# Performance work log

Hardware: AMD Instinct MI355X
Metric: run time of the kernel (lower is better)

The kernel has to match this reference:

```python
import jax, jax.numpy as jnp
import numpy as np
from jax import lax

B = 64
FEAT = 512
SEED_DIM = 128
NUM_PC = 256
NPART = 4096
NFPS = 512


def setup_inputs() -> dict:
    key = jax.random.key(0)
    ks = jax.random.split(key, 32)
    s = 0.02
    rn = lambda k, shape: jax.random.normal(k, shape, jnp.float32) * s
    inp = {}
    inp["feat"] = jax.random.normal(ks[0], (B, FEAT, 1), jnp.float32)
    inp["patch_xyz"] = jax.random.normal(ks[1], (B, 3, 128), jnp.float32)
    inp["patch_feat"] = jax.random.normal(ks[2], (B, FEAT, 128), jnp.float32)
    inp["partial"] = jax.random.normal(ks[3], (B, NPART, 3), jnp.float32)
    # ConvTranspose1d(512, 128, 256): weight [in, out, k]
    inp["ps_w"] = rn(ks[4], (FEAT, 128, NUM_PC))
    inp["ps_b"] = jnp.zeros((128,), jnp.float32)
    # MLP_Res(in, hidden, out): conv1 [hid,in], conv2 [out,hid], shortcut [out,in]
    def mlp_res_params(k, din, dhid, dout):
        k1, k2, k3 = jax.random.split(k, 3)
        return (rn(k1, (dhid, din)), jnp.zeros((dhid,), jnp.float32),
                rn(k2, (dout, dhid)), jnp.zeros((dout,), jnp.float32),
                rn(k3, (dout, din)), jnp.zeros((dout,), jnp.float32))
    (inp["m1_w1"], inp["m1_b1"], inp["m1_w2"], inp["m1_b2"], inp["m1_ws"], inp["m1_bs"]) = mlp_res_params(ks[5], FEAT + 128, 128, 128)
    (inp["m2_w1"], inp["m2_b1"], inp["m2_w2"], inp["m2_b2"], inp["m2_ws"], inp["m2_bs"]) = mlp_res_params(ks[6], 128, 64, 128)
    (inp["m3_w1"], inp["m3_b1"], inp["m3_w2"], inp["m3_b2"], inp["m3_ws"], inp["m3_bs"]) = mlp_res_params(ks[7], FEAT + 128, 128, SEED_DIM)
    inp["m4_w1"] = rn(ks[8], (64, SEED_DIM))
    inp["m4_b1"] = jnp.zeros((64,), jnp.float32)
    inp["m4_w2"] = rn(ks[9], (3, 64))
    inp["m4_b2"] = jnp.zeros((3,), jnp.float32)
    return inp


def _conv1(w, b, x):
    # 1x1 Conv1d: w [out,in], x [B,in,N] -> [B,out,N]
    return jnp.einsum('oi,bin->bon', w, x) + b[None, :, None]


def _mlp_res(x, w1, b1, w2, b2, ws, bs):
    h = jax.nn.relu(_conv1(w1, b1, x))
    return _conv1(w2, b2, h) + _conv1(ws, bs, x)


def _fps(xyz, npoint):
    # farthest point sampling (PointNet++ semantics, start at index 0)
    # xyz: [B, N, 3] -> [B, npoint, 3]
    Bb, N, _ = xyz.shape
    dist0 = jnp.full((Bb, N), 1e10, dtype=xyz.dtype)
    far0 = jnp.zeros((Bb,), jnp.int32)

    def step(carry, _):
        dist, far = carry
        centroid = jnp.take_along_axis(xyz, far[:, None, None], axis=1)  # [B,1,3]
        d = jnp.sum((xyz - centroid) ** 2, axis=-1)  # [B,N]
        dist = jnp.minimum(dist, d)
        new_far = jnp.argmax(dist, axis=-1).astype(jnp.int32)
        return (dist, new_far), far

    _, idxs = lax.scan(step, (dist0, far0), None, length=npoint)  # [npoint, B]
    idxs = idxs.T  # [B, npoint]
    return jnp.take_along_axis(xyz, idxs[..., None], axis=1)


def reference(feat, patch_xyz, patch_feat, partial,
              ps_w, ps_b,
              m1_w1, m1_b1, m1_w2, m1_b2, m1_ws, m1_bs,
              m2_w1, m2_b1, m2_w2, m2_b2, m2_ws, m2_bs,
              m3_w1, m3_b1, m3_w2, m3_b2, m3_ws, m3_bs,
              m4_w1, m4_b1, m4_w2, m4_b2):
    # ConvTranspose1d on length-1 input: [B,C,1] x [C,O,K] -> [B,O,K]
    x1 = jnp.einsum('bc,cok->bok', feat[:, :, 0], ps_w) + ps_b[None, :, None]
    feat_r = jnp.broadcast_to(feat, (feat.shape[0], feat.shape[1], NUM_PC))
    x1 = _mlp_res(jnp.concatenate([x1, feat_r], axis=1), m1_w1, m1_b1, m1_w2, m1_b2, m1_ws, m1_bs)
    x2 = _mlp_res(x1, m2_w1, m2_b1, m2_w2, m2_b2, m2_ws, m2_bs)
    x3 = _mlp_res(jnp.concatenate([x2, feat_r], axis=1), m3_w1, m3_b1, m3_w2, m3_b2, m3_ws, m3_bs)
    seed = _conv1(m4_w2, m4_b2, jax.nn.relu(_conv1(m4_w1, m4_b1, x3)))  # [B,3,256]
    all_pts = jnp.concatenate([seed.transpose(0, 2, 1), partial], axis=1)  # [B,256+N,3]
    x = _fps(all_pts, NFPS).transpose(0, 2, 1)  # [B,3,512]
    return (seed, x3, x)
```

## Files before the change

kernel.cpp:

```cpp
#include <hip/hip_runtime.h>
#include <stdint.h>

#define X3_OFF 49152
#define FPS_OFF 2146304


__global__ void k_prep(const float* __restrict__ feat, float* __restrict__ ws) {
    int g = blockIdx.x * 256 + threadIdx.x;
    int c = g >> 6, b = g & 63;
    ws[32768 + c * 64 + b] = feat[b * 512 + c];
}

__global__ void k_tterms(const float* __restrict__ w1, const float* __restrict__ ws1,
                         const float* __restrict__ w3, const float* __restrict__ ws3,
                         float* __restrict__ ws) {
    int g = blockIdx.x * 256 + threadIdx.x;
    int which = g >> 13;
    int o = (g >> 6) & 127;
    int b = g & 63;
    const float* W = (which == 0) ? w1 : (which == 1) ? ws1
                     : (which == 2) ? w3 : ws3;
    const float* ft = ws + 32768;
    float acc = 0.f;
#pragma unroll 4
    for (int c = 0; c < 512; ++c)
        acc = fmaf(W[o * 640 + 128 + c], ft[c * 64 + b], acc);
    ws[which * 8192 + o * 64 + b] = acc;
}

__global__ void k_deconv(const float* __restrict__ psw,
                         const float* __restrict__ psb,
                         const float* __restrict__ ws,
                         float* __restrict__ stage) {
    int n = blockIdx.x * 256 + threadIdx.x;
    int b0 = blockIdx.y * 16;
    const float* featT = ws + 32768;
    float acc[16];
    float bias = psb[n >> 8];
#pragma unroll
    for (int j = 0; j < 16; ++j) acc[j] = bias;
    for (int c = 0; c < 512; ++c) {
        float pw = psw[c * 32768 + n];
#pragma unroll
        for (int j = 0; j < 16; ++j)
            acc[j] = fmaf(pw, featT[c * 64 + b0 + j], acc[j]);
    }
#pragma unroll
    for (int j = 0; j < 16; ++j)
        stage[(b0 + j) * 32768 + n] = acc[j];
}

__device__ __forceinline__ void gemm8(const float* __restrict__ Wg, int ld, int o0,
                                      const float* S, int K, float acc[8], int lane) {
#pragma unroll 4
    for (int i = 0; i < K; ++i) {
        float x = S[i * 64 + lane];
#pragma unroll
        for (int r = 0; r < 8; ++r)
            acc[r] = fmaf(x, Wg[(o0 + r) * ld + i], acc[r]);
    }
}

struct FusedW {
    const float *m1_w1, *m1_b1, *m1_w2, *m1_b2, *m1_ws, *m1_bs;
    const float *m2_w1, *m2_b1, *m2_w2, *m2_b2, *m2_ws, *m2_bs;
    const float *m3_w1, *m3_b1, *m3_w2, *m3_b2, *m3_ws, *m3_bs;
    const float *m4_w1, *m4_b1, *m4_w2, *m4_b2;
};

__global__ void __launch_bounds__(512)
k_fused(FusedW P, const float* __restrict__ ws, float* __restrict__ fout) {
    int b  = blockIdx.x >> 2;
    int k0 = (blockIdx.x & 3) * 64;
    int lane = threadIdx.x & 63;
    int wave = __builtin_amdgcn_readfirstlane(threadIdx.x >> 6);

    const float* T1  = ws;
    const float* T1s = ws + 8192;
    const float* T3  = ws + 16384;
    const float* T3s = ws + 24576;
    float* stage = fout + X3_OFF + b * 32768;

    __shared__ float Xs[8192];
    __shared__ float Hs[8192];

#pragma unroll
    for (int s = 0; s < 16; ++s) {
        int e = threadIdx.x + s * 512;
        int o = e >> 6, kk = e & 63;
        Xs[e] = stage[o * 256 + k0 + kk];
    }
    __syncthreads();

    float yreg[2][8];

#pragma unroll
    for (int half = 0; half < 2; ++half) {
        int o0 = wave * 16 + half * 8;
        float acc[8];
#pragma unroll
        for (int r = 0; r < 8; ++r) acc[r] = T1[(o0 + r) * 64 + b] + P.m1_b1[o0 + r];
        gemm8(P.m1_w1, 640, o0, Xs, 128, acc, lane);
#pragma unroll
        for (int r = 0; r < 8; ++r) Hs[(o0 + r) * 64 + lane] = fmaxf(acc[r], 0.f);
    }
    __syncthreads();
#pragma unroll
    for (int half = 0; half < 2; ++half) {
        int o0 = wave * 16 + half * 8;
        float acc[8];
#pragma unroll
        for (int r = 0; r < 8; ++r)
            acc[r] = T1s[(o0 + r) * 64 + b] + P.m1_b2[o0 + r] + P.m1_bs[o0 + r];
        gemm8(P.m1_w2, 128, o0, Hs, 128, acc, lane);
        gemm8(P.m1_ws, 640, o0, Xs, 128, acc, lane);
#pragma unroll
        for (int r = 0; r < 8; ++r) yreg[half][r] = acc[r];
    }
    __syncthreads();
#pragma unroll
    for (int half = 0; half < 2; ++half) {
        int o0 = wave * 16 + half * 8;
#pragma unroll
        for (int r = 0; r < 8; ++r) Xs[(o0 + r) * 64 + lane] = yreg[half][r];
    }
    __syncthreads();

    {
        int o0 = wave * 8;
        float acc[8];
#pragma unroll
        for (int r = 0; r < 8; ++r) acc[r] = P.m2_b1[o0 + r];
        gemm8(P.m2_w1, 128, o0, Xs, 128, acc, lane);
#pragma unroll
        for (int r = 0; r < 8; ++r) Hs[(o0 + r) * 64 + lane] = fmaxf(acc[r], 0.f);
    }
    __syncthreads();
#pragma unroll
    for (int half = 0; half < 2; ++half) {
        int o0 = wave * 16 + half * 8;
        float acc[8];
#pragma unroll
        for (int r = 0; r < 8; ++r) acc[r] = P.m2_b2[o0 + r] + P.m2_bs[o0 + r];
        gemm8(P.m2_w2, 64, o0, Hs, 64, acc, lane);
        gemm8(P.m2_ws, 128, o0, Xs, 128, acc, lane);
#pragma unroll
        for (int r = 0; r < 8; ++r) yreg[half][r] = acc[r];
    }
    __syncthreads();
#pragma unroll
    for (int half = 0; half < 2; ++half) {
        int o0 = wave * 16 + half * 8;
#pragma unroll
        for (int r = 0; r < 8; ++r) Xs[(o0 + r) * 64 + lane] = yreg[half][r];
    }
    __syncthreads();

#pragma unroll
    for (int half = 0; half < 2; ++half) {
        int o0 = wave * 16 + half * 8;
        float acc[8];
#pragma unroll
        for (int r = 0; r < 8; ++r) acc[r] = T3[(o0 + r) * 64 + b] + P.m3_b1[o0 + r];
        gemm8(P.m3_w1, 640, o0, Xs, 128, acc, lane);
#pragma unroll
        for (int r = 0; r < 8; ++r) Hs[(o0 + r) * 64 + lane] = fmaxf(acc[r], 0.f);
    }
    __syncthreads();
#pragma unroll
    for (int half = 0; half < 2; ++half) {
        int o0 = wave * 16 + half * 8;
        float acc[8];
#pragma unroll
        for (int r = 0; r < 8; ++r)
            acc[r] = T3s[(o0 + r) * 64 + b] + P.m3_b2[o0 + r] + P.m3_bs[o0 + r];
        gemm8(P.m3_w2, 128, o0, Hs, 128, acc, lane);
        gemm8(P.m3_ws, 640, o0, Xs, 128, acc, lane);
#pragma unroll
        for (int r = 0; r < 8; ++r) yreg[half][r] = acc[r];
    }
    __syncthreads();
#pragma unroll
    for (int half = 0; half < 2; ++half) {
        int o0 = wave * 16 + half * 8;
#pragma unroll
        for (int r = 0; r < 8; ++r) {
            Xs[(o0 + r) * 64 + lane] = yreg[half][r];
            stage[(o0 + r) * 256 + k0 + lane] = yreg[half][r];
        }
    }
    __syncthreads();

    {
        int o0 = wave * 8;
        float acc[8];
#pragma unroll
        for (int r = 0; r < 8; ++r) acc[r] = P.m4_b1[o0 + r];
        gemm8(P.m4_w1, 128, o0, Xs, 128, acc, lane);
#pragma unroll
        for (int r = 0; r < 8; ++r) Hs[(o0 + r) * 64 + lane] = fmaxf(acc[r], 0.f);
    }
    __syncthreads();
    if (wave < 3) {
        int d = wave;
        float s = P.m4_b2[d];
        for (int j = 0; j < 64; ++j)
            s = fmaf(Hs[j * 64 + lane], P.m4_w2[d * 64 + j], s);
        fout[b * 768 + d * 256 + k0 + lane] = s;
    }
}

__device__ __forceinline__ unsigned wave_max_u32_l63(unsigned v) {
    unsigned t;
    t = (unsigned)__builtin_amdgcn_update_dpp(0, (int)v, 0x111, 0xf, 0xf, false); v = t > v ? t : v;
    t = (unsigned)__builtin_amdgcn_update_dpp(0, (int)v, 0x112, 0xf, 0xf, false); v = t > v ? t : v;
    t = (unsigned)__builtin_amdgcn_update_dpp(0, (int)v, 0x114, 0xf, 0xf, false); v = t > v ? t : v;
    t = (unsigned)__builtin_amdgcn_update_dpp(0, (int)v, 0x118, 0xf, 0xf, false); v = t > v ? t : v;
    t = (unsigned)__builtin_amdgcn_update_dpp(0, (int)v, 0x142, 0xa, 0xf, false); v = t > v ? t : v;
    t = (unsigned)__builtin_amdgcn_update_dpp(0, (int)v, 0x143, 0xc, 0xf, false); v = t > v ? t : v;
    return v;
}
__device__ __forceinline__ unsigned wave_min_u32_l63(unsigned v) {
    unsigned t;
    t = (unsigned)__builtin_amdgcn_update_dpp(-1, (int)v, 0x111, 0xf, 0xf, false); v = t < v ? t : v;
    t = (unsigned)__builtin_amdgcn_update_dpp(-1, (int)v, 0x112, 0xf, 0xf, false); v = t < v ? t : v;
    t = (unsigned)__builtin_amdgcn_update_dpp(-1, (int)v, 0x114, 0xf, 0xf, false); v = t < v ? t : v;
    t = (unsigned)__builtin_amdgcn_update_dpp(-1, (int)v, 0x118, 0xf, 0xf, false); v = t < v ? t : v;
    t = (unsigned)__builtin_amdgcn_update_dpp(-1, (int)v, 0x142, 0xa, 0xf, false); v = t < v ? t : v;
    t = (unsigned)__builtin_amdgcn_update_dpp(-1, (int)v, 0x143, 0xc, 0xf, false); v = t < v ? t : v;
    return v;
}

__device__ __forceinline__ unsigned umin_u(unsigned a, unsigned b) { return a < b ? a : b; }

__global__ void __launch_bounds__(256)
k_fps(const float* __restrict__ seed, const float* __restrict__ partial,
      float* __restrict__ outx) {
    int b = blockIdx.x;
    int tid = threadIdx.x;
    int lane = tid & 63;
    int wv = tid >> 6;

    __shared__ float pts[4352 * 3];
    __shared__ unsigned long long cand[2][4];
    __shared__ int fars[512];

    pts[tid * 3 + 0] = seed[b * 768 + tid];
    pts[tid * 3 + 1] = seed[b * 768 + 256 + tid];
    pts[tid * 3 + 2] = seed[b * 768 + 512 + tid];
#pragma unroll
    for (int j = 0; j < 48; ++j) {
        int e = tid + j * 256;
        pts[768 + e] = partial[b * 12288 + e];
    }
    if (tid == 0) fars[0] = 0;
    __syncthreads();

    float px[17], py[17], pz[17], dist[17];
#pragma unroll
    for (int s = 0; s < 17; ++s) {
        int g = s * 256 + tid;
        px[s] = pts[g * 3 + 0];
        py[s] = pts[g * 3 + 1];
        pz[s] = pts[g * 3 + 2];
        dist[s] = 1e10f;
    }
    float cx = pts[0], cy = pts[1], cz = pts[2];

    for (int t = 0; t < 511; ++t) {
#pragma unroll
        for (int s = 0; s < 17; ++s) {
            float dx = px[s] - cx, dy = py[s] - cy, dz = pz[s] - cz;
            float d = __fadd_rn(__fadd_rn(__fmul_rn(dx, dx), __fmul_rn(dy, dy)),
                                __fmul_rn(dz, dz));
            dist[s] = fminf(dist[s], d);
        }
        float a0 = fmaxf(fmaxf(dist[0], dist[1]), dist[2]);
        float a1 = fmaxf(fmaxf(dist[3], dist[4]), dist[5]);
        float a2 = fmaxf(fmaxf(dist[6], dist[7]), dist[8]);
        float a3 = fmaxf(fmaxf(dist[9], dist[10]), dist[11]);
        float a4 = fmaxf(fmaxf(dist[12], dist[13]), dist[14]);
        float a5 = fmaxf(dist[15], dist[16]);
        float b0 = fmaxf(fmaxf(a0, a1), a2);
        float b1 = fmaxf(fmaxf(a3, a4), a5);
        float m  = fmaxf(b0, b1);
        unsigned e[17];
#pragma unroll
        for (int s = 0; s < 17; ++s)
            e[s] = (dist[s] == m) ? (unsigned)s : 63u;
        unsigned c0 = umin_u(umin_u(e[0], e[1]), e[2]);
        unsigned c1 = umin_u(umin_u(e[3], e[4]), e[5]);
        unsigned c2 = umin_u(umin_u(e[6], e[7]), e[8]);
        unsigned c3 = umin_u(umin_u(e[9], e[10]), e[11]);
        unsigned c4 = umin_u(umin_u(e[12], e[13]), e[14]);
        unsigned c5 = umin_u(e[15], e[16]);
        unsigned d0 = umin_u(umin_u(c0, c1), c2);
        unsigned d1 = umin_u(umin_u(c3, c4), c5);
        unsigned sm = umin_u(d0, d1);
        unsigned bg = (sm << 8) + (unsigned)tid;

        unsigned mv = wave_max_u32_l63(__float_as_uint(m));
        unsigned maxbits = (unsigned)__builtin_amdgcn_readlane((int)mv, 63);
        unsigned cg = (__float_as_uint(m) == maxbits) ? bg : 0xFFFFFFFFu;
        unsigned mgv = wave_min_u32_l63(cg);
        unsigned big = (unsigned)__builtin_amdgcn_readlane((int)mgv, 63);

        if (lane == 0)
            cand[t & 1][wv] = (((unsigned long long)maxbits) << 32) |
                              (unsigned long long)(8191u - big);
        __syncthreads();
        unsigned long long U0 = cand[t & 1][0];
        unsigned long long U1 = cand[t & 1][1];
        unsigned long long U2 = cand[t & 1][2];
        unsigned long long U3 = cand[t & 1][3];
        if (U1 > U0) U0 = U1;
        if (U3 > U2) U2 = U3;
        if (U2 > U0) U0 = U2;
        int bi = 8191 - (int)(U0 & 8191ull);
        cx = pts[bi * 3 + 0]; cy = pts[bi * 3 + 1]; cz = pts[bi * 3 + 2];
        if (tid == 0) fars[t + 1] = bi;
    }
    __syncthreads();

#pragma unroll
    for (int j = 0; j < 2; ++j) {
        int n = tid + j * 256;
        int idx = fars[n];
        int ob = b * 1536 + n;
        outx[ob]        = pts[idx * 3 + 0];
        outx[ob + 512]  = pts[idx * 3 + 1];
        outx[ob + 1024] = pts[idx * 3 + 2];
    }
}

extern "C" void kernel_launch(void* const* d_in, const int* in_sizes, int n_in,
                              void* d_out, int out_size, void* d_ws, size_t ws_size,
                              hipStream_t stream) {
    (void)in_sizes; (void)n_in; (void)out_size; (void)ws_size;
    const float* feat    = (const float*)d_in[0];
    const float* partial = (const float*)d_in[3];
    const float* psw     = (const float*)d_in[4];
    const float* psb     = (const float*)d_in[5];

    FusedW P;
    P.m1_w1 = (const float*)d_in[6];  P.m1_b1 = (const float*)d_in[7];
    P.m1_w2 = (const float*)d_in[8];  P.m1_b2 = (const float*)d_in[9];
    P.m1_ws = (const float*)d_in[10]; P.m1_bs = (const float*)d_in[11];
    P.m2_w1 = (const float*)d_in[12]; P.m2_b1 = (const float*)d_in[13];
    P.m2_w2 = (const float*)d_in[14]; P.m2_b2 = (const float*)d_in[15];
    P.m2_ws = (const float*)d_in[16]; P.m2_bs = (const float*)d_in[17];
    P.m3_w1 = (const float*)d_in[18]; P.m3_b1 = (const float*)d_in[19];
    P.m3_w2 = (const float*)d_in[20]; P.m3_b2 = (const float*)d_in[21];
    P.m3_ws = (const float*)d_in[22]; P.m3_bs = (const float*)d_in[23];
    P.m4_w1 = (const float*)d_in[24]; P.m4_b1 = (const float*)d_in[25];
    P.m4_w2 = (const float*)d_in[26]; P.m4_b2 = (const float*)d_in[27];

    float* W = (float*)d_ws;
    float* out = (float*)d_out;

    k_prep<<<dim3(128), dim3(256), 0, stream>>>(feat, W);
    k_tterms<<<dim3(128), dim3(256), 0, stream>>>(P.m1_w1, P.m1_ws, P.m3_w1, P.m3_ws, W);
    k_deconv<<<dim3(128, 4), dim3(256), 0, stream>>>(psw, psb, W, out + X3_OFF);
    k_fused<<<dim3(256), dim3(512), 0, stream>>>(P, W, out);
    k_fps<<<dim3(64), dim3(256), 0, stream>>>(out, partial, out + FPS_OFF);
}
```

Measured before the change: 764.1 us.

## Merge prep and tterms kernels, widen deconv batch tile, simplify FPS argmax

Merges the feature transpose and the tterms GEMV into one launch, with tterms now reading feat directly so it no longer depends on the transposed copy. The deconv kernel now covers 32 batches per thread instead of 16, halving its grid and the repeated reads of the large ps_w weight, at the cost of more registers per thread. The FPS per-thread argmax is replaced by a running compare inside the distance loop rather than a max tree followed by an equality search. The FPS loop is sequential and likely dominates runtime, so the net effect depends mostly on that inner-loop change.

```diff
diff --git a/kernel.cpp b/kernel.cpp
--- a/kernel.cpp
+++ b/kernel.cpp
@@ -5,48 +5,51 @@
 #define FPS_OFF 2146304
 
 
-__global__ void k_prep(const float* __restrict__ feat, float* __restrict__ ws) {
-    int g = blockIdx.x * 256 + threadIdx.x;
-    int c = g >> 6, b = g & 63;
-    ws[32768 + c * 64 + b] = feat[b * 512 + c];
-}
-
-__global__ void k_tterms(const float* __restrict__ w1, const float* __restrict__ ws1,
-                         const float* __restrict__ w3, const float* __restrict__ ws3,
-                         float* __restrict__ ws) {
-    int g = blockIdx.x * 256 + threadIdx.x;
-    int which = g >> 13;
-    int o = (g >> 6) & 127;
-    int b = g & 63;
-    const float* W = (which == 0) ? w1 : (which == 1) ? ws1
-                     : (which == 2) ? w3 : ws3;
-    const float* ft = ws + 32768;
-    float acc = 0.f;
+__global__ void k_prep_tterms(const float* __restrict__ feat,
+                              const float* __restrict__ w1, const float* __restrict__ ws1,
+                              const float* __restrict__ w3, const float* __restrict__ ws3,
+                              float* __restrict__ ws) {
+    int blk = blockIdx.x;
+    if (blk < 128) {
+        int g = blk * 256 + threadIdx.x;
+        int c = g >> 6, b = g & 63;
+        ws[32768 + c * 64 + b] = feat[b * 512 + c];
+    } else {
+        int g = (blk - 128) * 256 + threadIdx.x;
+        int which = g >> 13;
+        int o = (g >> 6) & 127;
+        int b = g & 63;
+        const float* W = (which == 0) ? w1 : (which == 1) ? ws1
+                         : (which == 2) ? w3 : ws3;
+        float acc = 0.f;
 #pragma unroll 4
-    for (int c = 0; c < 512; ++c)
-        acc = fmaf(W[o * 640 + 128 + c], ft[c * 64 + b], acc);
-    ws[which * 8192 + o * 64 + b] = acc;
-}
-
-__global__ void k_deconv(const float* __restrict__ psw,
-                         const float* __restrict__ psb,
-                         const float* __restrict__ ws,
-                         float* __restrict__ stage) {
+        for (int c = 0; c < 512; ++c)
+            acc = fmaf(W[o * 640 + 128 + c], feat[b * 512 + c], acc);
+        ws[which * 8192 + o * 64 + b] = acc;
+    }
+}
+
+__global__ void __launch_bounds__(256)
+k_deconv(const float* __restrict__ psw,
+         const float* __restrict__ psb,
+         const float* __restrict__ ws,
+         float* __restrict__ stage) {
     int n = blockIdx.x * 256 + threadIdx.x;
-    int b0 = blockIdx.y * 16;
+    int b0 = blockIdx.y * 32;
     const float* featT = ws + 32768;
-    float acc[16];
+    float acc[32];
     float bias = psb[n >> 8];
 #pragma unroll
-    for (int j = 0; j < 16; ++j) acc[j] = bias;
+    for (int j = 0; j < 32; ++j) acc[j] = bias;
+#pragma unroll 2
     for (int c = 0; c < 512; ++c) {
         float pw = psw[c * 32768 + n];
 #pragma unroll
-        for (int j = 0; j < 16; ++j)
+        for (int j = 0; j < 32; ++j)
             acc[j] = fmaf(pw, featT[c * 64 + b0 + j], acc[j]);
     }
 #pragma unroll
-    for (int j = 0; j < 16; ++j)
+    for (int j = 0; j < 32; ++j)
         stage[(b0 + j) * 32768 + n] = acc[j];
 }
 
@@ -231,8 +234,6 @@
     return v;
 }
 
-__device__ __forceinline__ unsigned umin_u(unsigned a, unsigned b) { return a < b ? a : b; }
-
 __global__ void __launch_bounds__(256)
 k_fps(const float* __restrict__ seed, const float* __restrict__ partial,
       float* __restrict__ outx) {
@@ -268,40 +269,18 @@
     float cx = pts[0], cy = pts[1], cz = pts[2];
 
     for (int t = 0; t < 511; ++t) {
+        float bv = -1.0f; int bg = 0;
 #pragma unroll
         for (int s = 0; s < 17; ++s) {
             float dx = px[s] - cx, dy = py[s] - cy, dz = pz[s] - cz;
             float d = __fadd_rn(__fadd_rn(__fmul_rn(dx, dx), __fmul_rn(dy, dy)),
                                 __fmul_rn(dz, dz));
             dist[s] = fminf(dist[s], d);
+            if (dist[s] > bv) { bv = dist[s]; bg = s * 256 + tid; }
         }
-        float a0 = fmaxf(fmaxf(dist[0], dist[1]), dist[2]);
-        float a1 = fmaxf(fmaxf(dist[3], dist[4]), dist[5]);
-        float a2 = fmaxf(fmaxf(dist[6], dist[7]), dist[8]);
-        float a3 = fmaxf(fmaxf(dist[9], dist[10]), dist[11]);
-        float a4 = fmaxf(fmaxf(dist[12], dist[13]), dist[14]);
-        float a5 = fmaxf(dist[15], dist[16]);
-        float b0 = fmaxf(fmaxf(a0, a1), a2);
-        float b1 = fmaxf(fmaxf(a3, a4), a5);
-        float m  = fmaxf(b0, b1);
-        unsigned e[17];
-#pragma unroll
-        for (int s = 0; s < 17; ++s)
-            e[s] = (dist[s] == m) ? (unsigned)s : 63u;
-        unsigned c0 = umin_u(umin_u(e[0], e[1]), e[2]);
-        unsigned c1 = umin_u(umin_u(e[3], e[4]), e[5]);
-        unsigned c2 = umin_u(umin_u(e[6], e[7]), e[8]);
-        unsigned c3 = umin_u(umin_u(e[9], e[10]), e[11]);
-        unsigned c4 = umin_u(umin_u(e[12], e[13]), e[14]);
-        unsigned c5 = umin_u(e[15], e[16]);
-        unsigned d0 = umin_u(umin_u(c0, c1), c2);
-        unsigned d1 = umin_u(umin_u(c3, c4), c5);
-        unsigned sm = umin_u(d0, d1);
-        unsigned bg = (sm << 8) + (unsigned)tid;
-
-        unsigned mv = wave_max_u32_l63(__float_as_uint(m));
+        unsigned mv = wave_max_u32_l63(__float_as_uint(bv));
         unsigned maxbits = (unsigned)__builtin_amdgcn_readlane((int)mv, 63);
-        unsigned cg = (__float_as_uint(m) == maxbits) ? bg : 0xFFFFFFFFu;
+        unsigned cg = (__float_as_uint(bv) == maxbits) ? (unsigned)bg : 0xFFFFFFFFu;
         unsigned mgv = wave_min_u32_l63(cg);
         unsigned big = (unsigned)__builtin_amdgcn_readlane((int)mgv, 63);
 
@@ -358,9 +337,8 @@
     float* W = (float*)d_ws;
     float* out = (float*)d_out;
 
-    k_prep<<<dim3(128), dim3(256), 0, stream>>>(feat, W);
-    k_tterms<<<dim3(128), dim3(256), 0, stream>>>(P.m1_w1, P.m1_ws, P.m3_w1, P.m3_ws, W);
-    k_deconv<<<dim3(128, 4), dim3(256), 0, stream>>>(psw, psb, W, out + X3_OFF);
+    k_prep_tterms<<<dim3(256), dim3(256), 0, stream>>>(feat, P.m1_w1, P.m1_ws, P.m3_w1, P.m3_ws, W);
+    k_deconv<<<dim3(128, 2), dim3(256), 0, stream>>>(psw, psb, W, out + X3_OFF);
     k_fused<<<dim3(256), dim3(512), 0, stream>>>(P, W, out);
     k_fps<<<dim3(64), dim3(256), 0, stream>>>(out, partial, out + FPS_OFF);
 }
```

Result: no change. 749.4 us (-1.9%).
